# Kernel tuning notes

Measured on AMD Instinct MI355X. Metric: run time of the kernel, lower is better.

## Reference

```python
import jax, jax.numpy as jnp
import numpy as np

B, N, K = 32, 8192, 256   # batch_size, mux_in, mux_out
TEMP = 1.0                # Gumbel-softmax temperature
MEM_PENALTY = -1000.0     # penalty for already-sampled elements


def setup_inputs() -> dict:
    key = jax.random.key(0)
    k1, k2 = jax.random.split(key)
    logits = jax.random.normal(k1, (B, N), dtype=jnp.float32)
    # Gumbel(0,1) noise, one draw per (batch, mux_in), repeated over mux_out
    u = jax.random.uniform(k2, (B, N), dtype=jnp.float32, minval=1e-6, maxval=1.0 - 1e-6)
    noise = -jnp.log(-jnp.log(u))
    sample_memory = jnp.zeros((B, N), dtype=jnp.float32)
    return {"logits": logits, "noise": noise, "sample_memory": sample_memory}


def reference(logits, noise, sample_memory):
    # perturbed logits, identical across the K (mux_out) axis -> keep as [B, N]
    perturbed = logits + noise + sample_memory * MEM_PENALTY  # [B, N]

    # top-K selection (straight-through hard path)
    _, topk_idx = jax.lax.top_k(perturbed, K)  # [B, K]
    b_idx = jnp.arange(B)[:, None]             # [B, 1]
    k_idx = jnp.arange(K)[None, :]             # [1, K]

    hard = jnp.zeros((B, N), logits.dtype).at[b_idx, topk_idx].set(1.0)
    hard = hard + sample_memory                # [B, N]

    # masking_matrix: for column k, all elements picked at steps < k are -inf,
    # the element picked at step k is 0 (scatter -inf, cumsum over k, reset to 0)
    M = jnp.zeros((B, N, K), logits.dtype).at[b_idx, topk_idx, k_idx].set(-jnp.inf)
    M = jnp.cumsum(M, axis=2)
    M = M.at[b_idx, topk_idx, k_idx].set(0.0)  # [B, N, K]

    masked = perturbed[:, :, None] + M                         # [B, N, K]
    soft = jax.nn.softmax(masked / TEMP, axis=1).sum(axis=2)   # [B, N]

    # straight-through estimator
    return hard - jax.lax.stop_gradient(soft) + soft
```

## Files before the change

### kernel.cpp

```cpp
#include <hip/hip_runtime.h>


#define NROW 32
#define NCOL 8192
#define KSEL 256
#define THREADS 1024
#define H0S 4097

__device__ __forceinline__ unsigned float_to_key(float f) {
    unsigned u = __float_as_uint(f);
    return (u & 0x80000000u) ? ~u : (u | 0x80000000u);
}

__global__ __launch_bounds__(THREADS) void topk_kernel(
    const float* __restrict__ logits, const float* __restrict__ noise,
    const float* __restrict__ mem, float* __restrict__ out)
{
    __shared__ unsigned hist0[4 * H0S];
    __shared__ __align__(16) unsigned hist1[4096];
    __shared__ unsigned hist2[256];
    __shared__ unsigned wpart[16];
    __shared__ unsigned sh_pn[2];

    const int tid  = threadIdx.x;
    const int wave = tid >> 6;
    const int lane = tid & 63;
    const int grp  = wave >> 2;
    const int base = blockIdx.x * NCOL + tid * 8;

    float4 lg0 = ((const float4*)(logits + base))[0];
    float4 lg1 = ((const float4*)(logits + base))[1];
    float4 no0 = ((const float4*)(noise  + base))[0];
    float4 no1 = ((const float4*)(noise  + base))[1];
    float4 mm0 = ((const float4*)(mem    + base))[0];
    float4 mm1 = ((const float4*)(mem    + base))[1];

    unsigned key[8];
    key[0] = float_to_key(lg0.x + no0.x + mm0.x * -1000.0f);
    key[1] = float_to_key(lg0.y + no0.y + mm0.y * -1000.0f);
    key[2] = float_to_key(lg0.z + no0.z + mm0.z * -1000.0f);
    key[3] = float_to_key(lg0.w + no0.w + mm0.w * -1000.0f);
    key[4] = float_to_key(lg1.x + no1.x + mm1.x * -1000.0f);
    key[5] = float_to_key(lg1.y + no1.y + mm1.y * -1000.0f);
    key[6] = float_to_key(lg1.z + no1.z + mm1.z * -1000.0f);
    key[7] = float_to_key(lg1.w + no1.w + mm1.w * -1000.0f);

#pragma unroll
    for (int i = tid; i < 4 * H0S; i += THREADS) hist0[i] = 0u;
#pragma unroll
    for (int i = tid; i < 4096; i += THREADS) hist1[i] = 0u;
    if (tid < 256) hist2[tid] = 0u;
    __syncthreads();

    {
        unsigned* h0 = hist0 + grp * H0S;
#pragma unroll
        for (int i = 0; i < 8; ++i) atomicAdd(&h0[key[i] >> 20], 1u);
    }
    __syncthreads();

    unsigned need = KSEL;
    unsigned p12, p24;
    const int dbase = 4095 - 4 * tid;

    {
        unsigned c[4], tot = 0;
#pragma unroll
        for (int j = 0; j < 4; ++j) {
            const int d = dbase - j;
            c[j] = hist0[d] + hist0[H0S + d] + hist0[2 * H0S + d] + hist0[3 * H0S + d];
            tot += c[j];
        }
        unsigned s = tot;
#pragma unroll
        for (int off = 1; off < 64; off <<= 1) {
            unsigned nv = __shfl_up(s, off, 64);
            if (lane >= off) s += nv;
        }
        if (lane == 63) wpart[wave] = s;
        __syncthreads();
        unsigned add = 0;
        for (int w = 0; w < wave; ++w) add += wpart[w];
        unsigned cum = s + add - tot;
#pragma unroll
        for (int j = 0; j < 4; ++j) {
            unsigned nc = cum + c[j];
            if (nc >= need && cum < need) {
                sh_pn[0] = (unsigned)(dbase - j);
                sh_pn[1] = need - cum;
            }
            cum = nc;
        }
    }
    __syncthreads();
    p12 = sh_pn[0]; need = sh_pn[1];

#pragma unroll
    for (int i = 0; i < 8; ++i)
        if ((key[i] >> 20) == p12)
            atomicAdd(&hist1[(key[i] >> 8) & 4095u], 1u);
    __syncthreads();

    {
        uint4 v = *(const uint4*)&hist1[dbase - 3];
        unsigned c[4] = {v.w, v.z, v.y, v.x};
        unsigned tot = c[0] + c[1] + c[2] + c[3];
        unsigned s = tot;
#pragma unroll
        for (int off = 1; off < 64; off <<= 1) {
            unsigned nv = __shfl_up(s, off, 64);
            if (lane >= off) s += nv;
        }
        if (lane == 63) wpart[wave] = s;
        __syncthreads();
        unsigned add = 0;
        for (int w = 0; w < wave; ++w) add += wpart[w];
        unsigned cum = s + add - tot;
#pragma unroll
        for (int j = 0; j < 4; ++j) {
            unsigned nc = cum + c[j];
            if (nc >= need && cum < need) {
                sh_pn[0] = (unsigned)(dbase - j);
                sh_pn[1] = need - cum;
            }
            cum = nc;
        }
    }
    __syncthreads();
    p24 = (p12 << 12) | sh_pn[0]; need = sh_pn[1];

#pragma unroll
    for (int i = 0; i < 8; ++i)
        if ((key[i] >> 8) == p24)
            atomicAdd(&hist2[key[i] & 255u], 1u);
    __syncthreads();

    if (wave == 0) {
        const int d0 = 255 - 4 * lane;
        unsigned c0 = hist2[d0], c1 = hist2[d0 - 1],
                 c2 = hist2[d0 - 2], c3 = hist2[d0 - 3];
        unsigned tot = c0 + c1 + c2 + c3, s = tot;
#pragma unroll
        for (int off = 1; off < 64; off <<= 1) {
            unsigned nv = __shfl_up(s, off, 64);
            if (lane >= off) s += nv;
        }
        unsigned P = s - tot;
        unsigned cum0 = P + c0, cum1 = cum0 + c1, cum2 = cum1 + c2, cum3 = cum2 + c3;
        if (cum0 >= need && P < need)         { sh_pn[0] = (unsigned)d0;       sh_pn[1] = need - P;    }
        else if (cum1 >= need && cum0 < need) { sh_pn[0] = (unsigned)(d0 - 1); sh_pn[1] = need - cum0; }
        else if (cum2 >= need && cum1 < need) { sh_pn[0] = (unsigned)(d0 - 2); sh_pn[1] = need - cum1; }
        else if (cum3 >= need && cum2 < need) { sh_pn[0] = (unsigned)(d0 - 3); sh_pn[1] = need - cum2; }
    }
    __syncthreads();
    const unsigned T     = (p24 << 8) | sh_pn[0];
    const unsigned needF = sh_pn[1];

    unsigned local_eq = 0;
#pragma unroll
    for (int i = 0; i < 8; ++i) local_eq += (key[i] == T) ? 1u : 0u;
    unsigned s2 = local_eq;
#pragma unroll
    for (int off = 1; off < 64; off <<= 1) {
        unsigned nv = __shfl_up(s2, off, 64);
        if (lane >= off) s2 += nv;
    }
    if (lane == 63) wpart[wave] = s2;
    __syncthreads();
    unsigned rank = s2 - local_eq;
    for (int w = 0; w < wave; ++w) rank += wpart[w];

    float o[8];
#pragma unroll
    for (int i = 0; i < 8; ++i) {
        float sel;
        if (key[i] > T)       sel = 1.0f;
        else if (key[i] == T) { sel = (rank < needF) ? 1.0f : 0.0f; ++rank; }
        else                  sel = 0.0f;
        o[i] = sel;
    }
    o[0] += mm0.x; o[1] += mm0.y; o[2] += mm0.z; o[3] += mm0.w;
    o[4] += mm1.x; o[5] += mm1.y; o[6] += mm1.z; o[7] += mm1.w;
    ((float4*)(out + base))[0] = make_float4(o[0], o[1], o[2], o[3]);
    ((float4*)(out + base))[1] = make_float4(o[4], o[5], o[6], o[7]);
}

extern "C" void kernel_launch(void* const* d_in, const int* in_sizes, int n_in,
                              void* d_out, int out_size, void* d_ws, size_t ws_size,
                              hipStream_t stream) {
    const float* logits = (const float*)d_in[0];
    const float* noise  = (const float*)d_in[1];
    const float* mem    = (const float*)d_in[2];
    float* out = (float*)d_out;

    topk_kernel<<<NROW, THREADS, 0, stream>>>(logits, noise, mem, out);
}
```

Baseline: 63.90 us.

## Split row top-k into two kernels across 256 blocks with global keys

Replaces the single 32-block kernel (one 1024-thread block per row) with two kernels of 256 blocks each. The first computes keys into workspace and per-chunk 8-bit histograms; the second has 8 blocks per row redundantly reload the full row's keys, run 12-bit and 12-bit radix refinement, and each write its own 1024-element slice. This spreads the work over more compute units to address the low occupancy of only 32 blocks, at the cost of an extra launch, a global round-trip for keys, and redundant per-row selection work.

```diff
diff --git a/kernel.cpp b/kernel.cpp
--- a/kernel.cpp
+++ b/kernel.cpp
@@ -4,185 +4,200 @@
 #define NROW 32
 #define NCOL 8192
 #define KSEL 256
-#define THREADS 1024
-#define H0S 4097
 
 __device__ __forceinline__ unsigned float_to_key(float f) {
     unsigned u = __float_as_uint(f);
     return (u & 0x80000000u) ? ~u : (u | 0x80000000u);
 }
 
-__global__ __launch_bounds__(THREADS) void topk_kernel(
+__global__ __launch_bounds__(256) void k1(
     const float* __restrict__ logits, const float* __restrict__ noise,
+    const float* __restrict__ mem,
+    unsigned* __restrict__ keys, unsigned* __restrict__ ghist)
+{
+    __shared__ unsigned h[4][257];
+    const int tid  = threadIdx.x;
+    const int wave = tid >> 6;
+    const int base = blockIdx.x * 1024 + tid * 4;
+
+    float4 lg = *(const float4*)(logits + base);
+    float4 no = *(const float4*)(noise  + base);
+    float4 mm = *(const float4*)(mem    + base);
+
+    h[0][tid] = 0u; h[1][tid] = 0u; h[2][tid] = 0u; h[3][tid] = 0u;
+    if (tid < 4) h[tid][256] = 0u;
+
+    unsigned k0 = float_to_key(lg.x + no.x + mm.x * -1000.0f);
+    unsigned k1v = float_to_key(lg.y + no.y + mm.y * -1000.0f);
+    unsigned k2v = float_to_key(lg.z + no.z + mm.z * -1000.0f);
+    unsigned k3v = float_to_key(lg.w + no.w + mm.w * -1000.0f);
+
+    *(uint4*)(keys + base) = make_uint4(k0, k1v, k2v, k3v);
+
+    __syncthreads();
+    unsigned* hw = h[wave];
+    atomicAdd(&hw[k0  >> 24], 1u);
+    atomicAdd(&hw[k1v >> 24], 1u);
+    atomicAdd(&hw[k2v >> 24], 1u);
+    atomicAdd(&hw[k3v >> 24], 1u);
+    __syncthreads();
+
+    ghist[blockIdx.x * 256 + tid] =
+        h[0][tid] + h[1][tid] + h[2][tid] + h[3][tid];
+}
+
+__global__ __launch_bounds__(256) void k2(
+    const unsigned* __restrict__ keys, const unsigned* __restrict__ ghist,
     const float* __restrict__ mem, float* __restrict__ out)
 {
-    __shared__ unsigned hist0[4 * H0S];
-    __shared__ __align__(16) unsigned hist1[4096];
-    __shared__ unsigned hist2[256];
-    __shared__ unsigned wpart[16];
-    __shared__ unsigned sh_pn[2];
+    __shared__ unsigned hist[4096];
+    __shared__ unsigned wp[4];
+    __shared__ unsigned wp8[8][4];
+    __shared__ unsigned sh_d, sh_need;
 
     const int tid  = threadIdx.x;
     const int wave = tid >> 6;
     const int lane = tid & 63;
-    const int grp  = wave >> 2;
-    const int base = blockIdx.x * NCOL + tid * 8;
-
-    float4 lg0 = ((const float4*)(logits + base))[0];
-    float4 lg1 = ((const float4*)(logits + base))[1];
-    float4 no0 = ((const float4*)(noise  + base))[0];
-    float4 no1 = ((const float4*)(noise  + base))[1];
-    float4 mm0 = ((const float4*)(mem    + base))[0];
-    float4 mm1 = ((const float4*)(mem    + base))[1];
-
-    unsigned key[8];
-    key[0] = float_to_key(lg0.x + no0.x + mm0.x * -1000.0f);
-    key[1] = float_to_key(lg0.y + no0.y + mm0.y * -1000.0f);
-    key[2] = float_to_key(lg0.z + no0.z + mm0.z * -1000.0f);
-    key[3] = float_to_key(lg0.w + no0.w + mm0.w * -1000.0f);
-    key[4] = float_to_key(lg1.x + no1.x + mm1.x * -1000.0f);
-    key[5] = float_to_key(lg1.y + no1.y + mm1.y * -1000.0f);
-    key[6] = float_to_key(lg1.z + no1.z + mm1.z * -1000.0f);
-    key[7] = float_to_key(lg1.w + no1.w + mm1.w * -1000.0f);
-
-#pragma unroll
-    for (int i = tid; i < 4 * H0S; i += THREADS) hist0[i] = 0u;
-#pragma unroll
-    for (int i = tid; i < 4096; i += THREADS) hist1[i] = 0u;
-    if (tid < 256) hist2[tid] = 0u;
-    __syncthreads();
-
+    const int r = blockIdx.x >> 3;
+    const int s = blockIdx.x & 7;
+    const int rowbase = r * NCOL;
+
+    unsigned key[8][4];
+#pragma unroll
+    for (int j = 0; j < 8; ++j) {
+        uint4 v = *(const uint4*)(keys + rowbase + j * 1024 + tid * 4);
+        key[j][0] = v.x; key[j][1] = v.y; key[j][2] = v.z; key[j][3] = v.w;
+    }
+    float4 mm = *(const float4*)(mem + rowbase + s * 1024 + tid * 4);
+
+#pragma unroll
+    for (int i = tid; i < 4096; i += 256) hist[i] = 0u;
+
+    unsigned c = 0;
+#pragma unroll
+    for (int j = 0; j < 8; ++j) c += ghist[(r * 8 + j) * 256 + (255 - tid)];
+    unsigned sc = c;
+#pragma unroll
+    for (int off = 1; off < 64; off <<= 1) {
+        unsigned nv = __shfl_up(sc, off, 64);
+        if (lane >= off) sc += nv;
+    }
+    if (lane == 63) wp[wave] = sc;
+    __syncthreads();
     {
-        unsigned* h0 = hist0 + grp * H0S;
-#pragma unroll
-        for (int i = 0; i < 8; ++i) atomicAdd(&h0[key[i] >> 20], 1u);
-    }
-    __syncthreads();
-
-    unsigned need = KSEL;
-    unsigned p12, p24;
-    const int dbase = 4095 - 4 * tid;
-
+        unsigned add = 0;
+        for (int w = 0; w < wave; ++w) add += wp[w];
+        unsigned incl = sc + add, excl = incl - c;
+        if (incl >= KSEL && excl < KSEL) { sh_d = 255u - (unsigned)tid; sh_need = KSEL - excl; }
+    }
+    __syncthreads();
+    const unsigned b0 = sh_d;
+    unsigned need = sh_need;
+
+#pragma unroll
+    for (int j = 0; j < 8; ++j)
+#pragma unroll
+        for (int i = 0; i < 4; ++i)
+            if ((key[j][i] >> 24) == b0)
+                atomicAdd(&hist[(key[j][i] >> 12) & 4095u], 1u);
+    __syncthreads();
     {
-        unsigned c[4], tot = 0;
-#pragma unroll
-        for (int j = 0; j < 4; ++j) {
-            const int d = dbase - j;
-            c[j] = hist0[d] + hist0[H0S + d] + hist0[2 * H0S + d] + hist0[3 * H0S + d];
-            tot += c[j];
-        }
-        unsigned s = tot;
+        unsigned cc[16], tot = 0;
+#pragma unroll
+        for (int j2 = 0; j2 < 16; ++j2) { cc[j2] = hist[4095 - 16 * tid - j2]; tot += cc[j2]; }
+        unsigned s2 = tot;
 #pragma unroll
         for (int off = 1; off < 64; off <<= 1) {
-            unsigned nv = __shfl_up(s, off, 64);
-            if (lane >= off) s += nv;
-        }
-        if (lane == 63) wpart[wave] = s;
+            unsigned nv = __shfl_up(s2, off, 64);
+            if (lane >= off) s2 += nv;
+        }
+        if (lane == 63) wp[wave] = s2;
         __syncthreads();
         unsigned add = 0;
-        for (int w = 0; w < wave; ++w) add += wpart[w];
-        unsigned cum = s + add - tot;
-#pragma unroll
-        for (int j = 0; j < 4; ++j) {
-            unsigned nc = cum + c[j];
-            if (nc >= need && cum < need) {
-                sh_pn[0] = (unsigned)(dbase - j);
-                sh_pn[1] = need - cum;
-            }
+        for (int w = 0; w < wave; ++w) add += wp[w];
+        unsigned cum = s2 + add - tot;
+#pragma unroll
+        for (int j2 = 0; j2 < 16; ++j2) {
+            unsigned nc = cum + cc[j2];
+            if (nc >= need && cum < need) { sh_d = 4095u - 16u * tid - j2; sh_need = need - cum; }
             cum = nc;
         }
     }
     __syncthreads();
-    p12 = sh_pn[0]; need = sh_pn[1];
-
-#pragma unroll
-    for (int i = 0; i < 8; ++i)
-        if ((key[i] >> 20) == p12)
-            atomicAdd(&hist1[(key[i] >> 8) & 4095u], 1u);
-    __syncthreads();
-
+    const unsigned p20 = (b0 << 12) | sh_d;
+    need = sh_need;
+
+#pragma unroll
+    for (int i = tid; i < 4096; i += 256) hist[i] = 0u;
+    __syncthreads();
+#pragma unroll
+    for (int j = 0; j < 8; ++j)
+#pragma unroll
+        for (int i = 0; i < 4; ++i)
+            if ((key[j][i] >> 12) == p20)
+                atomicAdd(&hist[key[j][i] & 4095u], 1u);
+    __syncthreads();
     {
-        uint4 v = *(const uint4*)&hist1[dbase - 3];
-        unsigned c[4] = {v.w, v.z, v.y, v.x};
-        unsigned tot = c[0] + c[1] + c[2] + c[3];
-        unsigned s = tot;
+        unsigned cc[16], tot = 0;
+#pragma unroll
+        for (int j2 = 0; j2 < 16; ++j2) { cc[j2] = hist[4095 - 16 * tid - j2]; tot += cc[j2]; }
+        unsigned s2 = tot;
 #pragma unroll
         for (int off = 1; off < 64; off <<= 1) {
-            unsigned nv = __shfl_up(s, off, 64);
-            if (lane >= off) s += nv;
-        }
-        if (lane == 63) wpart[wave] = s;
+            unsigned nv = __shfl_up(s2, off, 64);
+            if (lane >= off) s2 += nv;
+        }
+        if (lane == 63) wp[wave] = s2;
         __syncthreads();
         unsigned add = 0;
-        for (int w = 0; w < wave; ++w) add += wpart[w];
-        unsigned cum = s + add - tot;
-#pragma unroll
-        for (int j = 0; j < 4; ++j) {
-            unsigned nc = cum + c[j];
-            if (nc >= need && cum < need) {
-                sh_pn[0] = (unsigned)(dbase - j);
-                sh_pn[1] = need - cum;
-            }
+        for (int w = 0; w < wave; ++w) add += wp[w];
+        unsigned cum = s2 + add - tot;
+#pragma unroll
+        for (int j2 = 0; j2 < 16; ++j2) {
+            unsigned nc = cum + cc[j2];
+            if (nc >= need && cum < need) { sh_d = 4095u - 16u * tid - j2; sh_need = need - cum; }
             cum = nc;
         }
     }
     __syncthreads();
-    p24 = (p12 << 12) | sh_pn[0]; need = sh_pn[1];
-
-#pragma unroll
-    for (int i = 0; i < 8; ++i)
-        if ((key[i] >> 8) == p24)
-            atomicAdd(&hist2[key[i] & 255u], 1u);
-    __syncthreads();
-
-    if (wave == 0) {
-        const int d0 = 255 - 4 * lane;
-        unsigned c0 = hist2[d0], c1 = hist2[d0 - 1],
-                 c2 = hist2[d0 - 2], c3 = hist2[d0 - 3];
-        unsigned tot = c0 + c1 + c2 + c3, s = tot;
+    const unsigned T     = (p20 << 12) | sh_d;
+    const unsigned needF = sh_need;
+
+    unsigned e[8], pfx[8];
+#pragma unroll
+    for (int j = 0; j < 8; ++j) {
+        unsigned cnt = 0;
+#pragma unroll
+        for (int i = 0; i < 4; ++i) cnt += (key[j][i] == T) ? 1u : 0u;
+        e[j] = cnt;
+        unsigned ss = cnt;
 #pragma unroll
         for (int off = 1; off < 64; off <<= 1) {
-            unsigned nv = __shfl_up(s, off, 64);
-            if (lane >= off) s += nv;
-        }
-        unsigned P = s - tot;
-        unsigned cum0 = P + c0, cum1 = cum0 + c1, cum2 = cum1 + c2, cum3 = cum2 + c3;
-        if (cum0 >= need && P < need)         { sh_pn[0] = (unsigned)d0;       sh_pn[1] = need - P;    }
-        else if (cum1 >= need && cum0 < need) { sh_pn[0] = (unsigned)(d0 - 1); sh_pn[1] = need - cum0; }
-        else if (cum2 >= need && cum1 < need) { sh_pn[0] = (unsigned)(d0 - 2); sh_pn[1] = need - cum1; }
-        else if (cum3 >= need && cum2 < need) { sh_pn[0] = (unsigned)(d0 - 3); sh_pn[1] = need - cum2; }
-    }
-    __syncthreads();
-    const unsigned T     = (p24 << 8) | sh_pn[0];
-    const unsigned needF = sh_pn[1];
-
-    unsigned local_eq = 0;
-#pragma unroll
-    for (int i = 0; i < 8; ++i) local_eq += (key[i] == T) ? 1u : 0u;
-    unsigned s2 = local_eq;
-#pragma unroll
-    for (int off = 1; off < 64; off <<= 1) {
-        unsigned nv = __shfl_up(s2, off, 64);
-        if (lane >= off) s2 += nv;
-    }
-    if (lane == 63) wpart[wave] = s2;
-    __syncthreads();
-    unsigned rank = s2 - local_eq;
-    for (int w = 0; w < wave; ++w) rank += wpart[w];
-
-    float o[8];
-#pragma unroll
-    for (int i = 0; i < 8; ++i) {
+            unsigned nv = __shfl_up(ss, off, 64);
+            if (lane >= off) ss += nv;
+        }
+        if (lane == 63) wp8[j][wave] = ss;
+        pfx[j] = ss - cnt;
+    }
+    __syncthreads();
+    unsigned rank = 0;
+    for (int j = 0; j < s; ++j)
+        rank += wp8[j][0] + wp8[j][1] + wp8[j][2] + wp8[j][3];
+    rank += pfx[s];
+    for (int w = 0; w < wave; ++w) rank += wp8[s][w];
+
+    float o[4];
+#pragma unroll
+    for (int i = 0; i < 4; ++i) {
+        unsigned k = key[s][i];
         float sel;
-        if (key[i] > T)       sel = 1.0f;
-        else if (key[i] == T) { sel = (rank < needF) ? 1.0f : 0.0f; ++rank; }
-        else                  sel = 0.0f;
+        if (k > T)       sel = 1.0f;
+        else if (k == T) { sel = (rank < needF) ? 1.0f : 0.0f; ++rank; }
+        else             sel = 0.0f;
         o[i] = sel;
     }
-    o[0] += mm0.x; o[1] += mm0.y; o[2] += mm0.z; o[3] += mm0.w;
-    o[4] += mm1.x; o[5] += mm1.y; o[6] += mm1.z; o[7] += mm1.w;
-    ((float4*)(out + base))[0] = make_float4(o[0], o[1], o[2], o[3]);
-    ((float4*)(out + base))[1] = make_float4(o[4], o[5], o[6], o[7]);
+    o[0] += mm.x; o[1] += mm.y; o[2] += mm.z; o[3] += mm.w;
+    *(float4*)(out + rowbase + s * 1024 + tid * 4) = make_float4(o[0], o[1], o[2], o[3]);
 }
 
 extern "C" void kernel_launch(void* const* d_in, const int* in_sizes, int n_in,
@@ -193,5 +208,9 @@
     const float* mem    = (const float*)d_in[2];
     float* out = (float*)d_out;
 
-    topk_kernel<<<NROW, THREADS, 0, stream>>>(logits, noise, mem, out);
-}
+    unsigned* keys  = (unsigned*)d_ws;
+    unsigned* ghist = (unsigned*)((char*)d_ws + NROW * NCOL * 4);
+
+    k1<<<256, 256, 0, stream>>>(logits, noise, mem, keys, ghist);
+    k2<<<256, 256, 0, stream>>>(keys, ghist, mem, out);
+}
```

Measured after the change: 69.97 us. 1.1x slower.

## Split each row's top-k across eight cooperating blocks with global flag sync

Applied to the files above, without the earlier changes.

Launches 256 blocks of 256 threads instead of 32 blocks of 1024, so each row's 8192 elements are spread over eight blocks. Each block builds a local radix histogram and publishes a coarse 256-bin version to workspace. Blocks of the same row then sync through spin-waited magic-value flags, and each block finds the top-byte pivot. Candidates in the pivot bucket are exchanged through global memory and refined in LDS, with tie ranks resolved by column index. The aim is to fill many more CUs. The cost is inter-block spin-waits and flags that are never reset between calls, so later launches may read stale sync state. It also depends on all 256 blocks being co-resident and on the workspace being large enough.

```diff
diff --git a/kernel.cpp b/kernel.cpp
--- a/kernel.cpp
+++ b/kernel.cpp
@@ -4,15 +4,238 @@
 #define NROW 32
 #define NCOL 8192
 #define KSEL 256
-#define THREADS 1024
-#define H0S 4097
+#define MAGIC1 0x51A7E001u
+#define MAGIC2 0x51A7E002u
+
+#define GHIST_OFF 0u
+#define CCNT_OFF  65536u
+#define F1_OFF    66048u
+#define F2_OFF    74240u
+#define CP_OFF    82432u
+#define WS_REQ_BYTES ((82432u + 524288u) * 4u)
 
 __device__ __forceinline__ unsigned float_to_key(float f) {
     unsigned u = __float_as_uint(f);
     return (u & 0x80000000u) ? ~u : (u | 0x80000000u);
 }
 
-__global__ __launch_bounds__(THREADS) void topk_kernel(
+__global__ __launch_bounds__(256) void fused_topk(
+    const float* __restrict__ logits, const float* __restrict__ noise,
+    const float* __restrict__ mem, float* __restrict__ out,
+    unsigned* __restrict__ ws)
+{
+    __shared__ unsigned hist[4096];
+    __shared__ uint2    cand[8192];
+    __shared__ unsigned wp[4];
+    __shared__ unsigned sh_d, sh_need;
+    __shared__ unsigned cnt_sh[8];
+
+    unsigned* ghist = ws + GHIST_OFF;
+    unsigned* ccnt  = ws + CCNT_OFF;
+    unsigned* fl1   = ws + F1_OFF;
+    unsigned* fl2   = ws + F2_OFF;
+    uint2*    cpairs = (uint2*)(ws + CP_OFF);
+
+    const int tid  = threadIdx.x;
+    const int wave = tid >> 6;
+    const int lane = tid & 63;
+    const int r   = blockIdx.x >> 3;
+    const int s   = blockIdx.x & 7;
+    const int seg = r * 8 + s;
+    const int gbase = r * NCOL + s * 1024 + tid * 4;
+
+    float4 lg = *(const float4*)(logits + gbase);
+    float4 no = *(const float4*)(noise  + gbase);
+    float4 mm = *(const float4*)(mem    + gbase);
+
+    for (int i = tid; i < 4096; i += 256) hist[i] = 0u;
+
+    unsigned key[4];
+    key[0] = float_to_key(lg.x + no.x + mm.x * -1000.0f);
+    key[1] = float_to_key(lg.y + no.y + mm.y * -1000.0f);
+    key[2] = float_to_key(lg.z + no.z + mm.z * -1000.0f);
+    key[3] = float_to_key(lg.w + no.w + mm.w * -1000.0f);
+    __syncthreads();
+
+#pragma unroll
+    for (int i = 0; i < 4; ++i) atomicAdd(&hist[key[i] >> 20], 1u);
+    __syncthreads();
+
+    {
+        unsigned csum = 0;
+#pragma unroll
+        for (int j = 0; j < 16; ++j) csum += hist[tid * 16 + j];
+        ghist[seg * 256 + tid] = csum;
+    }
+    __threadfence();
+    __syncthreads();
+    if (tid == 0) atomicExch(&fl1[seg * 32], MAGIC1);
+    if (tid < 8) {
+        while (atomicAdd(&fl1[(r * 8 + tid) * 32], 0u) != MAGIC1)
+            __builtin_amdgcn_s_sleep(2);
+    }
+    __syncthreads();
+    __threadfence();
+
+    unsigned c = 0;
+    {
+        const unsigned* gh = ghist + r * 8 * 256;
+#pragma unroll
+        for (int j = 0; j < 8; ++j) c += gh[j * 256 + (255 - tid)];
+    }
+    {
+        unsigned sc = c;
+#pragma unroll
+        for (int off = 1; off < 64; off <<= 1) {
+            unsigned nv = __shfl_up(sc, off, 64);
+            if (lane >= off) sc += nv;
+        }
+        if (lane == 63) wp[wave] = sc;
+        __syncthreads();
+        unsigned add = 0;
+        for (int w = 0; w < wave; ++w) add += wp[w];
+        unsigned incl = sc + add, excl = incl - c;
+        if (incl >= KSEL && excl < KSEL) { sh_d = 255u - (unsigned)tid; sh_need = KSEL - excl; }
+    }
+    __syncthreads();
+    const unsigned b0 = sh_d;
+    unsigned need = sh_need;
+
+    unsigned mc = 0;
+#pragma unroll
+    for (int i = 0; i < 4; ++i) mc += ((key[i] >> 24) == b0) ? 1u : 0u;
+    {
+        unsigned ss = mc;
+#pragma unroll
+        for (int off = 1; off < 64; off <<= 1) {
+            unsigned nv = __shfl_up(ss, off, 64);
+            if (lane >= off) ss += nv;
+        }
+        if (lane == 63) wp[wave] = ss;
+        __syncthreads();
+        unsigned add = 0;
+        for (int w = 0; w < wave; ++w) add += wp[w];
+        unsigned myoff = ss + add - mc;
+        uint2* cp = cpairs + ((size_t)seg << 10);
+#pragma unroll
+        for (int i = 0; i < 4; ++i) {
+            if ((key[i] >> 24) == b0) {
+                cp[myoff] = make_uint2(key[i], (unsigned)(s * 1024 + tid * 4 + i));
+                ++myoff;
+            }
+        }
+        if (tid == 0) ccnt[seg] = wp[0] + wp[1] + wp[2] + wp[3];
+    }
+    __threadfence();
+    __syncthreads();
+    if (tid == 0) atomicExch(&fl2[seg * 32], MAGIC2);
+    if (tid < 8) {
+        while (atomicAdd(&fl2[(r * 8 + tid) * 32], 0u) != MAGIC2)
+            __builtin_amdgcn_s_sleep(2);
+    }
+    __syncthreads();
+    __threadfence();
+
+    if (tid < 8) cnt_sh[tid] = ccnt[r * 8 + tid];
+    __syncthreads();
+    unsigned coff[9];
+    coff[0] = 0;
+#pragma unroll
+    for (int j = 0; j < 8; ++j) coff[j + 1] = coff[j] + cnt_sh[j];
+    const unsigned total = coff[8];
+    for (int j = 0; j < 8; ++j) {
+        const uint2* cp = cpairs + ((size_t)(r * 8 + j) << 10);
+        for (unsigned i = tid; i < cnt_sh[j]; i += 256)
+            cand[coff[j] + i] = cp[i];
+    }
+    for (int i = tid; i < 4096; i += 256) hist[i] = 0u;
+    __syncthreads();
+
+    for (unsigned i = tid; i < total; i += 256)
+        atomicAdd(&hist[(cand[i].x >> 12) & 4095u], 1u);
+    __syncthreads();
+    {
+        unsigned cc[16], tot = 0;
+        const int tb = 4095 - 16 * tid;
+#pragma unroll
+        for (int j = 0; j < 16; ++j) { cc[j] = hist[tb - j]; tot += cc[j]; }
+        unsigned s2 = tot;
+#pragma unroll
+        for (int off = 1; off < 64; off <<= 1) {
+            unsigned nv = __shfl_up(s2, off, 64);
+            if (lane >= off) s2 += nv;
+        }
+        if (lane == 63) wp[wave] = s2;
+        __syncthreads();
+        unsigned add = 0;
+        for (int w = 0; w < wave; ++w) add += wp[w];
+        unsigned cum = s2 + add - tot;
+#pragma unroll
+        for (int j = 0; j < 16; ++j) {
+            unsigned nc = cum + cc[j];
+            if (nc >= need && cum < need) { sh_d = (unsigned)(tb - j); sh_need = need - cum; }
+            cum = nc;
+        }
+    }
+    __syncthreads();
+    const unsigned p24 = (b0 << 12) | sh_d;
+    need = sh_need;
+    for (int i = tid; i < 4096; i += 256) hist[i] = 0u;
+    __syncthreads();
+
+    for (unsigned i = tid; i < total; i += 256)
+        if ((cand[i].x >> 12) == p24)
+            atomicAdd(&hist[cand[i].x & 4095u], 1u);
+    __syncthreads();
+    {
+        unsigned cc[16], tot = 0;
+        const int tb = 4095 - 16 * tid;
+#pragma unroll
+        for (int j = 0; j < 16; ++j) { cc[j] = hist[tb - j]; tot += cc[j]; }
+        unsigned s2 = tot;
+#pragma unroll
+        for (int off = 1; off < 64; off <<= 1) {
+            unsigned nv = __shfl_up(s2, off, 64);
+            if (lane >= off) s2 += nv;
+        }
+        if (lane == 63) wp[wave] = s2;
+        __syncthreads();
+        unsigned add = 0;
+        for (int w = 0; w < wave; ++w) add += wp[w];
+        unsigned cum = s2 + add - tot;
+#pragma unroll
+        for (int j = 0; j < 16; ++j) {
+            unsigned nc = cum + cc[j];
+            if (nc >= need && cum < need) { sh_d = (unsigned)(tb - j); sh_need = need - cum; }
+            cum = nc;
+        }
+    }
+    __syncthreads();
+    const unsigned T     = (p24 << 12) | sh_d;
+    const unsigned needF = sh_need;
+
+    float o[4];
+#pragma unroll
+    for (int i = 0; i < 4; ++i) {
+        const unsigned k = key[i];
+        float sel = 0.0f;
+        if (k > T) {
+            sel = 1.0f;
+        } else if (k == T) {
+            const unsigned col = (unsigned)(s * 1024 + tid * 4 + i);
+            unsigned rk = 0;
+            for (unsigned q = 0; q < total; ++q)
+                rk += (cand[q].x == T && cand[q].y < col) ? 1u : 0u;
+            sel = (rk < needF) ? 1.0f : 0.0f;
+        }
+        o[i] = sel;
+    }
+    o[0] += mm.x; o[1] += mm.y; o[2] += mm.z; o[3] += mm.w;
+    *(float4*)(out + gbase) = make_float4(o[0], o[1], o[2], o[3]);
+}
+
+#define H0S 4097
+__global__ __launch_bounds__(1024) void topk_single32(
     const float* __restrict__ logits, const float* __restrict__ noise,
     const float* __restrict__ mem, float* __restrict__ out)
 {
@@ -45,10 +268,8 @@
     key[6] = float_to_key(lg1.z + no1.z + mm1.z * -1000.0f);
     key[7] = float_to_key(lg1.w + no1.w + mm1.w * -1000.0f);
 
-#pragma unroll
-    for (int i = tid; i < 4 * H0S; i += THREADS) hist0[i] = 0u;
-#pragma unroll
-    for (int i = tid; i < 4096; i += THREADS) hist1[i] = 0u;
+    for (int i = tid; i < 4 * H0S; i += 1024) hist0[i] = 0u;
+    for (int i = tid; i < 4096; i += 1024) hist1[i] = 0u;
     if (tid < 256) hist2[tid] = 0u;
     __syncthreads();
 
@@ -62,7 +283,6 @@
     unsigned need = KSEL;
     unsigned p12, p24;
     const int dbase = 4095 - 4 * tid;
-
     {
         unsigned c[4], tot = 0;
 #pragma unroll
@@ -85,10 +305,7 @@
 #pragma unroll
         for (int j = 0; j < 4; ++j) {
             unsigned nc = cum + c[j];
-            if (nc >= need && cum < need) {
-                sh_pn[0] = (unsigned)(dbase - j);
-                sh_pn[1] = need - cum;
-            }
+            if (nc >= need && cum < need) { sh_pn[0] = (unsigned)(dbase - j); sh_pn[1] = need - cum; }
             cum = nc;
         }
     }
@@ -100,7 +317,6 @@
         if ((key[i] >> 20) == p12)
             atomicAdd(&hist1[(key[i] >> 8) & 4095u], 1u);
     __syncthreads();
-
     {
         uint4 v = *(const uint4*)&hist1[dbase - 3];
         unsigned c[4] = {v.w, v.z, v.y, v.x};
@@ -119,10 +335,7 @@
 #pragma unroll
         for (int j = 0; j < 4; ++j) {
             unsigned nc = cum + c[j];
-            if (nc >= need && cum < need) {
-                sh_pn[0] = (unsigned)(dbase - j);
-                sh_pn[1] = need - cum;
-            }
+            if (nc >= need && cum < need) { sh_pn[0] = (unsigned)(dbase - j); sh_pn[1] = need - cum; }
             cum = nc;
         }
     }
@@ -193,5 +406,9 @@
     const float* mem    = (const float*)d_in[2];
     float* out = (float*)d_out;
 
-    topk_kernel<<<NROW, THREADS, 0, stream>>>(logits, noise, mem, out);
+    if (ws_size >= WS_REQ_BYTES) {
+        fused_topk<<<256, 256, 0, stream>>>(logits, noise, mem, out, (unsigned*)d_ws);
+    } else {
+        topk_single32<<<NROW, 1024, 0, stream>>>(logits, noise, mem, out);
+    }
 }
```

Measured after the change: 214.6 us. 3.36x slower.

## Replace second and third radix passes with candidate compaction and rank counting

Applied to the files above, without the earlier changes.

After the first 12-bit histogram pass, elements in the pivot bucket are compacted into shared memory with their column indices. Each such element then computes its exact rank by scanning all candidates, and this replaces the two later histogram/scan passes and the tie-rank scan. The change removes several barriers and prefix scans, cuts the histogram copies from four to two, and overlaps the histogram zeroing with the global loads. In exchange, the candidate loop is quadratic in the bucket size and will be slow if many keys land in the pivot bucket.

```diff
diff --git a/kernel.cpp b/kernel.cpp
--- a/kernel.cpp
+++ b/kernel.cpp
@@ -16,16 +16,16 @@
     const float* __restrict__ logits, const float* __restrict__ noise,
     const float* __restrict__ mem, float* __restrict__ out)
 {
-    __shared__ unsigned hist0[4 * H0S];
-    __shared__ __align__(16) unsigned hist1[4096];
-    __shared__ unsigned hist2[256];
-    __shared__ unsigned wpart[16];
-    __shared__ unsigned sh_pn[2];
+    __shared__ unsigned h0[2 * H0S];
+    __shared__ unsigned keyC[8192];
+    __shared__ unsigned short colC[8192];
+    __shared__ unsigned wp[16];
+    __shared__ unsigned sh_d, sh_need, sh_cnt;
 
     const int tid  = threadIdx.x;
     const int wave = tid >> 6;
     const int lane = tid & 63;
-    const int grp  = wave >> 2;
+    const int grp  = wave >> 3;
     const int base = blockIdx.x * NCOL + tid * 8;
 
     float4 lg0 = ((const float4*)(logits + base))[0];
@@ -34,6 +34,8 @@
     float4 no1 = ((const float4*)(noise  + base))[1];
     float4 mm0 = ((const float4*)(mem    + base))[0];
     float4 mm1 = ((const float4*)(mem    + base))[1];
+
+    for (int i = tid; i < 2 * H0S; i += THREADS) h0[i] = 0u;
 
     unsigned key[8];
     key[0] = float_to_key(lg0.x + no0.x + mm0.x * -1000.0f);
@@ -44,31 +46,23 @@
     key[5] = float_to_key(lg1.y + no1.y + mm1.y * -1000.0f);
     key[6] = float_to_key(lg1.z + no1.z + mm1.z * -1000.0f);
     key[7] = float_to_key(lg1.w + no1.w + mm1.w * -1000.0f);
-
-#pragma unroll
-    for (int i = tid; i < 4 * H0S; i += THREADS) hist0[i] = 0u;
-#pragma unroll
-    for (int i = tid; i < 4096; i += THREADS) hist1[i] = 0u;
-    if (tid < 256) hist2[tid] = 0u;
     __syncthreads();
 
     {
-        unsigned* h0 = hist0 + grp * H0S;
+        unsigned* h = h0 + grp * H0S;
 #pragma unroll
-        for (int i = 0; i < 8; ++i) atomicAdd(&h0[key[i] >> 20], 1u);
+        for (int i = 0; i < 8; ++i) atomicAdd(&h[key[i] >> 20], 1u);
     }
     __syncthreads();
 
     unsigned need = KSEL;
-    unsigned p12, p24;
-    const int dbase = 4095 - 4 * tid;
-
+    const int tb = 4095 - 4 * tid;
     {
         unsigned c[4], tot = 0;
 #pragma unroll
         for (int j = 0; j < 4; ++j) {
-            const int d = dbase - j;
-            c[j] = hist0[d] + hist0[H0S + d] + hist0[2 * H0S + d] + hist0[3 * H0S + d];
+            const int d = tb - j;
+            c[j] = h0[d] + h0[H0S + d];
             tot += c[j];
         }
         unsigned s = tot;
@@ -77,106 +71,52 @@
             unsigned nv = __shfl_up(s, off, 64);
             if (lane >= off) s += nv;
         }
-        if (lane == 63) wpart[wave] = s;
+        if (lane == 63) wp[wave] = s;
+        if (tid == 0) sh_cnt = 0u;
         __syncthreads();
         unsigned add = 0;
-        for (int w = 0; w < wave; ++w) add += wpart[w];
+        for (int w = 0; w < wave; ++w) add += wp[w];
         unsigned cum = s + add - tot;
 #pragma unroll
         for (int j = 0; j < 4; ++j) {
-            unsigned nc = cum + c[j];
-            if (nc >= need && cum < need) {
-                sh_pn[0] = (unsigned)(dbase - j);
-                sh_pn[1] = need - cum;
-            }
+            const unsigned nc = cum + c[j];
+            if (nc >= need && cum < need) { sh_d = (unsigned)(tb - j); sh_need = need - cum; }
             cum = nc;
         }
     }
     __syncthreads();
-    p12 = sh_pn[0]; need = sh_pn[1];
+    const unsigned p12 = sh_d;
+    need = sh_need;
 
 #pragma unroll
-    for (int i = 0; i < 8; ++i)
-        if ((key[i] >> 20) == p12)
-            atomicAdd(&hist1[(key[i] >> 8) & 4095u], 1u);
-    __syncthreads();
-
-    {
-        uint4 v = *(const uint4*)&hist1[dbase - 3];
-        unsigned c[4] = {v.w, v.z, v.y, v.x};
-        unsigned tot = c[0] + c[1] + c[2] + c[3];
-        unsigned s = tot;
-#pragma unroll
-        for (int off = 1; off < 64; off <<= 1) {
-            unsigned nv = __shfl_up(s, off, 64);
-            if (lane >= off) s += nv;
-        }
-        if (lane == 63) wpart[wave] = s;
-        __syncthreads();
-        unsigned add = 0;
-        for (int w = 0; w < wave; ++w) add += wpart[w];
-        unsigned cum = s + add - tot;
-#pragma unroll
-        for (int j = 0; j < 4; ++j) {
-            unsigned nc = cum + c[j];
-            if (nc >= need && cum < need) {
-                sh_pn[0] = (unsigned)(dbase - j);
-                sh_pn[1] = need - cum;
-            }
-            cum = nc;
+    for (int i = 0; i < 8; ++i) {
+        if ((key[i] >> 20) == p12) {
+            const unsigned slot = atomicAdd(&sh_cnt, 1u);
+            keyC[slot] = key[i];
+            colC[slot] = (unsigned short)(tid * 8 + i);
         }
     }
     __syncthreads();
-    p24 = (p12 << 12) | sh_pn[0]; need = sh_pn[1];
-
-#pragma unroll
-    for (int i = 0; i < 8; ++i)
-        if ((key[i] >> 8) == p24)
-            atomicAdd(&hist2[key[i] & 255u], 1u);
-    __syncthreads();
-
-    if (wave == 0) {
-        const int d0 = 255 - 4 * lane;
-        unsigned c0 = hist2[d0], c1 = hist2[d0 - 1],
-                 c2 = hist2[d0 - 2], c3 = hist2[d0 - 3];
-        unsigned tot = c0 + c1 + c2 + c3, s = tot;
-#pragma unroll
-        for (int off = 1; off < 64; off <<= 1) {
-            unsigned nv = __shfl_up(s, off, 64);
-            if (lane >= off) s += nv;
-        }
-        unsigned P = s - tot;
-        unsigned cum0 = P + c0, cum1 = cum0 + c1, cum2 = cum1 + c2, cum3 = cum2 + c3;
-        if (cum0 >= need && P < need)         { sh_pn[0] = (unsigned)d0;       sh_pn[1] = need - P;    }
-        else if (cum1 >= need && cum0 < need) { sh_pn[0] = (unsigned)(d0 - 1); sh_pn[1] = need - cum0; }
-        else if (cum2 >= need && cum1 < need) { sh_pn[0] = (unsigned)(d0 - 2); sh_pn[1] = need - cum1; }
-        else if (cum3 >= need && cum2 < need) { sh_pn[0] = (unsigned)(d0 - 3); sh_pn[1] = need - cum2; }
-    }
-    __syncthreads();
-    const unsigned T     = (p24 << 8) | sh_pn[0];
-    const unsigned needF = sh_pn[1];
-
-    unsigned local_eq = 0;
-#pragma unroll
-    for (int i = 0; i < 8; ++i) local_eq += (key[i] == T) ? 1u : 0u;
-    unsigned s2 = local_eq;
-#pragma unroll
-    for (int off = 1; off < 64; off <<= 1) {
-        unsigned nv = __shfl_up(s2, off, 64);
-        if (lane >= off) s2 += nv;
-    }
-    if (lane == 63) wpart[wave] = s2;
-    __syncthreads();
-    unsigned rank = s2 - local_eq;
-    for (int w = 0; w < wave; ++w) rank += wpart[w];
+    const unsigned M = sh_cnt;
 
     float o[8];
 #pragma unroll
     for (int i = 0; i < 8; ++i) {
+        const unsigned k = key[i];
         float sel;
-        if (key[i] > T)       sel = 1.0f;
-        else if (key[i] == T) { sel = (rank < needF) ? 1.0f : 0.0f; ++rank; }
-        else                  sel = 0.0f;
+        if ((k >> 20) > p12) {
+            sel = 1.0f;
+        } else if ((k >> 20) == p12) {
+            const unsigned short mycol = (unsigned short)(tid * 8 + i);
+            unsigned rk = 0;
+            for (unsigned q = 0; q < M; ++q) {
+                const unsigned kq = keyC[q];
+                rk += (kq > k || (kq == k && colC[q] < mycol)) ? 1u : 0u;
+            }
+            sel = (rk < need) ? 1.0f : 0.0f;
+        } else {
+            sel = 0.0f;
+        }
         o[i] = sel;
     }
     o[0] += mm0.x; o[1] += mm0.y; o[2] += mm0.z; o[3] += mm0.w;
```

Result: slower. 119.1 us (+86.3%).
